# Kernel optimization log

Hardware: AMD Instinct MI355X
Metric: run time of the kernel (lower is better)

Reference implementation:

```python
import jax, jax.numpy as jnp
import numpy as np
import math

B, C, N = 8, 128, 16384
H = 4
DK = C // H
COUT = 128
EPS = 1e-5

def _ln(x, g, b):
    # x: (B,H,N,DK); g,b: (H,DK) -> per-head LayerNorm over last dim
    mu = jnp.mean(x, axis=-1, keepdims=True)
    var = jnp.mean((x - mu) ** 2, axis=-1, keepdims=True)
    xh = (x - mu) / jnp.sqrt(var + EPS)
    return xh * g[None, :, None, :] + b[None, :, None, :]

def setup_inputs() -> dict:
    key = jax.random.key(0)
    ks = jax.random.split(key, 12)
    s = 0.02
    return {
        "x": jax.random.normal(ks[0], (B, C, N), jnp.float32),
        "Wq": jax.random.normal(ks[1], (C, C), jnp.float32) * s + 0.01 * jnp.eye(C),
        "bq": jnp.zeros((C,), jnp.float32),
        "Wk": jax.random.normal(ks[2], (C, C), jnp.float32) * s + 0.01 * jnp.eye(C),
        "bk": jnp.zeros((C,), jnp.float32),
        "Wv": jax.random.normal(ks[3], (C, C), jnp.float32) * s + 0.01 * jnp.eye(C),
        "bv": jnp.zeros((C,), jnp.float32),
        "gK": jnp.ones((H, DK), jnp.float32),
        "bK": jnp.zeros((H, DK), jnp.float32),
        "gV": jnp.ones((H, DK), jnp.float32),
        "bV": jnp.zeros((H, DK), jnp.float32),
        "Wo": jax.random.normal(ks[4], (COUT, C), jnp.float32) * s,
        "bo": jnp.zeros((COUT,), jnp.float32),
    }

def reference(x, Wq, bq, Wk, bk, Wv, bv, gK, bK, gV, bV, Wo, bo):
    # x: (B, C, N) -> (B, N, C)
    xt = jnp.transpose(x, (0, 2, 1))
    def proj(W, b):
        y = xt @ W.T + b                      # (B,N,C)
        return jnp.transpose(y.reshape(B, N, H, DK), (0, 2, 1, 3))  # (B,H,N,DK)
    q = proj(Wq, bq)
    k = proj(Wk, bk)
    v = proj(Wv, bv)
    # galerkin: per-head LayerNorm on K and V (vectorized over heads)
    k = _ln(k, gK, bK)
    v = _ln(v, gV, bV)
    # linear (no-softmax) attention: (Q K^T / sqrt(dk)) / N @ V == Q @ (K^T V) / (sqrt(dk)*N)
    # dropout from F.dropout is treated as identity (deterministic reference)
    kv = jnp.einsum("bhnd,bhne->bhde", k, v)            # (B,H,DK,DK)
    attn = jnp.einsum("bhnd,bhde->bhne", q, kv) / (math.sqrt(DK) * N)
    out = jnp.transpose(attn, (0, 2, 1, 3)).reshape(B, N, C)  # merge heads
    out = out @ Wo.T + bo                                # (B,N,COUT)
    return jnp.transpose(out, (0, 2, 1))                 # (B,COUT,N)
```

## Files before the change

### kernel.cpp

```cpp
#include <hip/hip_runtime.h>
#include <cmath>

#define BB 8
#define CC 128
#define NN 16384
#define HH 4
#define TN 64
#define NT2 (NN / TN)
#define NBK 64
#define SX 272

typedef __attribute__((ext_vector_type(8))) short bf16x8;
typedef __attribute__((ext_vector_type(4))) float f32x4;

#define MFMA(a, b, c) __builtin_amdgcn_mfma_f32_16x16x32_bf16(a, b, c, 0, 0, 0)

__device__ __forceinline__ unsigned short f2b(float f) {
  union { float f; unsigned u; } v; v.f = f;
  unsigned r = v.u + 0x7FFFu + ((v.u >> 16) & 1u);
  return (unsigned short)(r >> 16);
}

__device__ __forceinline__ int xt_addr(int n, int cblk) {
  return n * SX + ((cblk ^ ((n >> 2) & 7)) << 4);
}
__device__ __forceinline__ int kt_byte(int c, int n) {
  return c * 144 + ((((n >> 3) ^ (c & 7)) << 4) | ((n & 7) << 1));
}

__global__ void k_prep(const float* __restrict__ Wq, const float* __restrict__ Wk,
                       const float* __restrict__ Wv, const float* __restrict__ Wo,
                       unsigned short* __restrict__ Wb) {
  const int idx = blockIdx.x * 256 + threadIdx.x;
  const int which = idx >> 14;
  const float* src = (which == 0) ? Wq : (which == 1) ? Wk : (which == 2) ? Wv : Wo;
  Wb[idx] = f2b(src[idx & 16383]);
}

__global__ __launch_bounds__(512, 4)
void k_fuse1(const float* __restrict__ x,
             const unsigned short* __restrict__ Wkb, const unsigned short* __restrict__ Wvb,
             const float* __restrict__ bk, const float* __restrict__ bv,
             const float* __restrict__ gK, const float* __restrict__ bK,
             const float* __restrict__ gV, const float* __restrict__ bV,
             float* __restrict__ kvp) {
  extern __shared__ char lds[];
  char* XT = lds;
  char* KT = lds + 34816;
  char* VT = lds + 53248;
  float* KVS = (float*)lds;

  const int tid = threadIdx.x;
  const int lane = tid & 63;
  const int w = tid >> 6;
  const int b = blockIdx.y;
  const int bx = blockIdx.x;
  const int l15 = lane & 15, l4 = lane >> 4;

  const int ph = w >> 1, pp = w & 1;
  const int kh = w >> 1, khalf = w & 1;

  const unsigned short* Wsrc = pp ? Wvb : Wkb;
  bf16x8 wf[2][4];
#pragma unroll
  for (int mf = 0; mf < 2; ++mf)
#pragma unroll
    for (int ks = 0; ks < 4; ++ks)
      wf[mf][ks] = *(const bf16x8*)(Wsrc + (ph * 32 + mf * 16 + l15) * 128 + ks * 32 + l4 * 8);

  float bias[2][4], gam[2][4], bet[2][4];
  {
    const float* bsrc = pp ? bv : bk;
    const float* gsrc = pp ? gV : gK;
    const float* esrc = pp ? bV : bK;
#pragma unroll
    for (int mf = 0; mf < 2; ++mf)
#pragma unroll
      for (int r = 0; r < 4; ++r) {
        const int cg = ph * 32 + mf * 16 + l4 * 4 + r;
        bias[mf][r] = bsrc[cg]; gam[mf][r] = gsrc[cg]; bet[mf][r] = esrc[cg];
      }
  }

  f32x4 kvacc[2][2];
#pragma unroll
  for (int i = 0; i < 2; ++i)
#pragma unroll
    for (int j = 0; j < 2; ++j) kvacc[i][j] = (f32x4){0.f, 0.f, 0.f, 0.f};

  for (int ot = 0; ot < 2; ++ot) {
    const int n0 = (bx * 2 + ot) * 128;

#pragma unroll
    for (int g = 0; g < 2; ++g) {
      const int cb = w * 2 + g;
      const float* xb = x + ((size_t)b * CC + cb * 8) * NN + n0 + lane * 2;
      float2 va[8];
#pragma unroll
      for (int cc = 0; cc < 8; ++cc) va[cc] = *(const float2*)(xb + (size_t)cc * NN);
#pragma unroll
      for (int j = 0; j < 2; ++j) {
        const int n = lane * 2 + j;
        bf16x8 pk;
#pragma unroll
        for (int cc = 0; cc < 8; ++cc)
          ((unsigned short*)&pk)[cc] = f2b(j ? va[cc].y : va[cc].x);
        *(bf16x8*)(XT + n * SX + ((cb ^ ((n >> 2) & 7)) << 4)) = pk;
      }
    }
    __syncthreads();

    for (int t = 0; t < 2; ++t) {
      const int nbase = t * 64;
      char* DST = pp ? VT : KT;
#pragma unroll
      for (int nf = 0; nf < 4; ++nf) {
        const int n = nbase + nf * 16 + l15;
        f32x4 a0 = (f32x4){0.f, 0.f, 0.f, 0.f}, a1 = (f32x4){0.f, 0.f, 0.f, 0.f};
#pragma unroll
        for (int ks = 0; ks < 4; ++ks) {
          const bf16x8 xf = *(const bf16x8*)(XT + xt_addr(n, ks * 4 + l4));
          a0 = MFMA(wf[0][ks], xf, a0);
          a1 = MFMA(wf[1][ks], xf, a1);
        }
#pragma unroll
        for (int r = 0; r < 4; ++r) { a0[r] += bias[0][r]; a1[r] += bias[1][r]; }
        float s = 0.f, ss = 0.f;
#pragma unroll
        for (int r = 0; r < 4; ++r) {
          s += a0[r] + a1[r];
          ss += a0[r] * a0[r] + a1[r] * a1[r];
        }
        s += __shfl_xor(s, 16); ss += __shfl_xor(ss, 16);
        s += __shfl_xor(s, 32); ss += __shfl_xor(ss, 32);
        const float mu = s * (1.f / 32.f);
        const float var = ss * (1.f / 32.f) - mu * mu;
        const float rstd = rsqrtf(var + 1e-5f);
        const int nloc = nf * 16 + l15;
#pragma unroll
        for (int r = 0; r < 4; ++r) {
          const int c0k = ph * 32 + l4 * 4 + r;
          *(unsigned short*)(DST + kt_byte(c0k, nloc)) =
              f2b((a0[r] - mu) * rstd * gam[0][r] + bet[0][r]);
          const int c1k = ph * 32 + 16 + l4 * 4 + r;
          *(unsigned short*)(DST + kt_byte(c1k, nloc)) =
              f2b((a1[r] - mu) * rstd * gam[1][r] + bet[1][r]);
        }
      }
      __syncthreads();

#pragma unroll
      for (int mf = 0; mf < 2; ++mf) {
        const int ck = kh * 32 + mf * 16 + l15;
        const bf16x8 ka = *(const bf16x8*)(KT + ck * 144 + (((khalf * 4 + l4) ^ (ck & 7)) << 4));
#pragma unroll
        for (int ef = 0; ef < 2; ++ef) {
          const int cv = kh * 32 + ef * 16 + l15;
          const bf16x8 vb = *(const bf16x8*)(VT + cv * 144 + (((khalf * 4 + l4) ^ (cv & 7)) << 4));
          kvacc[mf][ef] = MFMA(ka, vb, kvacc[mf][ef]);
        }
      }
      __syncthreads();
    }
  }

#pragma unroll
  for (int mf = 0; mf < 2; ++mf)
#pragma unroll
    for (int ef = 0; ef < 2; ++ef)
#pragma unroll
      for (int r = 0; r < 4; ++r) {
        const int d = mf * 16 + l4 * 4 + r, e = ef * 16 + l15;
        KVS[w * 1024 + d * 32 + e] = kvacc[mf][ef][r];
      }
  __syncthreads();
  {
    float* og = kvp + ((size_t)(b * NBK + bx)) * 8192;
#pragma unroll
    for (int i = 0; i < 4; ++i) {
      const int off = i * 2048 + tid * 4;
      *(f32x4*)(og + off) = *(const f32x4*)(KVS + off);
    }
  }
}

__global__ void k_reduceA(const float* __restrict__ kvp, float* __restrict__ p2) {
  const int blk = blockIdx.x;
  const int s = blk & 7, h = (blk >> 3) & 3, b = blk >> 5;
  const int t = threadIdx.x;
  f32x4 acc = (f32x4){0.f, 0.f, 0.f, 0.f};
  for (int i = 0; i < 8; ++i) {
    const int bx = s * 8 + i;
    const float* base = kvp + ((size_t)(b * NBK + bx)) * 8192 + t * 4;
    acc += *(const f32x4*)(base + (2 * h) * 1024);
    acc += *(const f32x4*)(base + (2 * h + 1) * 1024);
  }
  *(f32x4*)(p2 + (size_t)blk * 1024 + t * 4) = acc;
}

__global__ void k_reduceB(const float* __restrict__ p2, unsigned short* __restrict__ kvT,
                          const float scale) {
  const int bh = blockIdx.x;
  const int t = threadIdx.x;
  f32x4 acc = (f32x4){0.f, 0.f, 0.f, 0.f};
  for (int s = 0; s < 8; ++s)
    acc += *(const f32x4*)(p2 + ((size_t)bh * 8 + s) * 1024 + t * 4);
#pragma unroll
  for (int j = 0; j < 4; ++j) {
    const int i = t * 4 + j;
    const int d = i >> 5, e = i & 31;
    kvT[(size_t)bh * 1024 + e * 32 + d] = f2b(acc[j] * scale);
  }
}

__global__ __launch_bounds__(512, 4)
void k_pass2(const float* __restrict__ x,
             const unsigned short* __restrict__ Wqb, const float* __restrict__ bq,
             const unsigned short* __restrict__ kvT,
             const unsigned short* __restrict__ Wob, const float* __restrict__ bo,
             float* __restrict__ out) {
  extern __shared__ char lds[];
  char* XT = lds;
  char* QS = lds + 17408;
  char* AS = lds + 33792;
  float* OS = (float*)lds;

  const int tid = threadIdx.x;
  const int lane = tid & 63;
  const int w = tid >> 6;
  const int b = blockIdx.y;
  const int n0 = blockIdx.x * TN;
  const int l15 = lane & 15, l4 = lane >> 4;
  const int h = w >> 1, half = w & 1;

  bf16x8 kvf[2];
#pragma unroll
  for (int mf = 0; mf < 2; ++mf)
    kvf[mf] = *(const bf16x8*)(kvT + (((size_t)b * HH + h) * 32 + mf * 16 + l15) * 32 + l4 * 8);
  bf16x8 wq[4], wo[4];
#pragma unroll
  for (int ks = 0; ks < 4; ++ks) {
    wq[ks] = *(const bf16x8*)(Wqb + (w * 16 + l15) * 128 + ks * 32 + l4 * 8);
    wo[ks] = *(const bf16x8*)(Wob + (w * 16 + l15) * 128 + ks * 32 + l4 * 8);
  }
  float bq_r[4], bo_r[4];
#pragma unroll
  for (int r = 0; r < 4; ++r) {
    bq_r[r] = bq[w * 16 + l4 * 4 + r];
    bo_r[r] = bo[w * 16 + l4 * 4 + r];
  }

#pragma unroll
  for (int p = 0; p < 2; ++p) {
    const int cb = p * 8 + w;
    const float* xb = x + ((size_t)b * CC + cb * 8) * NN + n0 + lane;
    float va[8];
#pragma unroll
    for (int cc = 0; cc < 8; ++cc) va[cc] = xb[(size_t)cc * NN];
    bf16x8 pk;
#pragma unroll
    for (int cc = 0; cc < 8; ++cc) ((unsigned short*)&pk)[cc] = f2b(va[cc]);
    *(bf16x8*)(XT + lane * SX + ((cb ^ ((lane >> 2) & 7)) << 4)) = pk;
  }
  __syncthreads();

  f32x4 qa[4];
#pragma unroll
  for (int nf = 0; nf < 4; ++nf) qa[nf] = (f32x4){0.f, 0.f, 0.f, 0.f};
#pragma unroll
  for (int ks = 0; ks < 4; ++ks)
#pragma unroll
    for (int nf = 0; nf < 4; ++nf) {
      const int n = nf * 16 + l15;
      const bf16x8 xf = *(const bf16x8*)(XT + xt_addr(n, ks * 4 + l4));
      qa[nf] = MFMA(wq[ks], xf, qa[nf]);
    }
#pragma unroll
  for (int nf = 0; nf < 4; ++nf) {
    const int n = nf * 16 + l15;
    const int c0 = w * 16 + l4 * 4;
    unsigned long long pk = 0;
#pragma unroll
    for (int r = 0; r < 4; ++r)
      pk |= (unsigned long long)f2b(qa[nf][r] + bq_r[r]) << (16 * r);
    *(unsigned long long*)(QS + n * 256 + (((c0 >> 3) ^ (n & 15)) << 4) + ((c0 & 7) << 1)) = pk;
  }
  __syncthreads();

  f32x4 aa[2][2];
#pragma unroll
  for (int i = 0; i < 2; ++i)
#pragma unroll
    for (int j = 0; j < 2; ++j) aa[i][j] = (f32x4){0.f, 0.f, 0.f, 0.f};
  bf16x8 qf[2];
#pragma unroll
  for (int nf = 0; nf < 2; ++nf) {
    const int n = half * 32 + nf * 16 + l15;
    const int cq = h * 32 + l4 * 8;
    qf[nf] = *(const bf16x8*)(QS + n * 256 + ((((cq >> 3)) ^ (n & 15)) << 4));
  }
#pragma unroll
  for (int mf = 0; mf < 2; ++mf)
#pragma unroll
    for (int nf = 0; nf < 2; ++nf) aa[mf][nf] = MFMA(kvf[mf], qf[nf], aa[mf][nf]);
#pragma unroll
  for (int mf = 0; mf < 2; ++mf)
#pragma unroll
    for (int nf = 0; nf < 2; ++nf) {
      const int n = half * 32 + nf * 16 + l15;
      const int e0 = h * 32 + mf * 16 + l4 * 4;
      unsigned long long pk = 0;
#pragma unroll
      for (int r = 0; r < 4; ++r)
        pk |= (unsigned long long)f2b(aa[mf][nf][r]) << (16 * r);
      *(unsigned long long*)(AS + n * 256 + (((e0 >> 3) ^ (n & 15)) << 4) + ((e0 & 7) << 1)) = pk;
    }
  __syncthreads();

  f32x4 oa[4];
#pragma unroll
  for (int nf = 0; nf < 4; ++nf) oa[nf] = (f32x4){0.f, 0.f, 0.f, 0.f};
#pragma unroll
  for (int ks = 0; ks < 4; ++ks)
#pragma unroll
    for (int nf = 0; nf < 4; ++nf) {
      const int n = nf * 16 + l15;
      const bf16x8 af = *(const bf16x8*)(AS + n * 256 + (((ks * 4 + l4) ^ (n & 15)) << 4));
      oa[nf] = MFMA(wo[ks], af, oa[nf]);
    }
#pragma unroll
  for (int nf = 0; nf < 4; ++nf)
#pragma unroll
    for (int r = 0; r < 4; ++r)
      OS[(w * 16 + l4 * 4 + r) * 64 + nf * 16 + l15] = oa[nf][r] + bo_r[r];
  __syncthreads();

  {
    const int c = tid >> 2, seg = (tid & 3) * 16;
    const float* srcp = OS + c * 64 + seg;
    float* dstp = out + (size_t)b * CC * NN + (size_t)c * NN + n0 + seg;
#pragma unroll
    for (int j = 0; j < 4; ++j)
      ((float4*)dstp)[j] = ((const float4*)srcp)[j];
  }
}

extern "C" void kernel_launch(void* const* d_in, const int* in_sizes, int n_in,
                              void* d_out, int out_size, void* d_ws, size_t ws_size,
                              hipStream_t stream) {
  const float* x  = (const float*)d_in[0];
  const float* Wq = (const float*)d_in[1];
  const float* bq = (const float*)d_in[2];
  const float* Wk = (const float*)d_in[3];
  const float* bk = (const float*)d_in[4];
  const float* Wv = (const float*)d_in[5];
  const float* bv = (const float*)d_in[6];
  const float* gK = (const float*)d_in[7];
  const float* bK = (const float*)d_in[8];
  const float* gV = (const float*)d_in[9];
  const float* bV = (const float*)d_in[10];
  const float* Wo = (const float*)d_in[11];
  const float* bo = (const float*)d_in[12];
  float* out = (float*)d_out;

  char* ws = (char*)d_ws;
  float* kvp = (float*)ws;
  float* p2  = kvp + (size_t)BB * NBK * 8192;
  unsigned short* kvTb = (unsigned short*)(p2 + 256 * 1024);
  unsigned short* Wb = kvTb + (size_t)BB * HH * 1024;
  const unsigned short* Wqb = Wb;
  const unsigned short* Wkb = Wb + 16384;
  const unsigned short* Wvb = Wb + 32768;
  const unsigned short* Wob = Wb + 49152;

  (void)hipFuncSetAttribute(reinterpret_cast<const void*>(k_fuse1),
                            hipFuncAttributeMaxDynamicSharedMemorySize, 71680);
  (void)hipFuncSetAttribute(reinterpret_cast<const void*>(k_pass2),
                            hipFuncAttributeMaxDynamicSharedMemorySize, 50176);

  k_prep<<<256, 256, 0, stream>>>(Wq, Wk, Wv, Wo, Wb);

  k_fuse1<<<dim3(NBK, BB), 512, 71680, stream>>>(
      x, Wkb, Wvb, bk, bv, gK, bK, gV, bV, kvp);

  k_reduceA<<<256, 256, 0, stream>>>(kvp, p2);

  const float scale = 1.0f / (5.65685424949238f * 16384.0f);
  k_reduceB<<<32, 256, 0, stream>>>(p2, kvTb, scale);

  k_pass2<<<dim3(NT2, BB), 512, 50176, stream>>>(
      x, Wqb, bq, kvTb, Wob, bo, out);
}
```

Before: 87.96 us.

## Register-prefetch x tiles with double-buffered LDS in fuse1 and persistent pass2

Both k_fuse1 and k_pass2 now loop over four 64-column tiles per block, loading the next tile of x into registers while the current one is converted and computed, and alternating between two LDS staging buffers. k_pass2 moves from 256 blocks per batch at 64 columns to 64 blocks at 256 columns, and it writes the output straight from MFMA registers rather than staging it through LDS for coalesced float4 stores. The goal is to hide global load latency and cut barriers and per-block setup. The cost is fewer blocks, more LDS per block, and output stores that are less coalesced.

```diff
diff --git a/kernel.cpp b/kernel.cpp
--- a/kernel.cpp
+++ b/kernel.cpp
@@ -5,8 +5,6 @@
 #define CC 128
 #define NN 16384
 #define HH 4
-#define TN 64
-#define NT2 (NN / TN)
 #define NBK 64
 #define SX 272
 
@@ -45,7 +43,6 @@
              const float* __restrict__ gV, const float* __restrict__ bV,
              float* __restrict__ kvp) {
   extern __shared__ char lds[];
-  char* XT = lds;
   char* KT = lds + 34816;
   char* VT = lds + 53248;
   float* KVS = (float*)lds;
@@ -88,82 +85,84 @@
 #pragma unroll
     for (int j = 0; j < 2; ++j) kvacc[i][j] = (f32x4){0.f, 0.f, 0.f, 0.f};
 
-  for (int ot = 0; ot < 2; ++ot) {
-    const int n0 = (bx * 2 + ot) * 128;
-
-#pragma unroll
-    for (int g = 0; g < 2; ++g) {
-      const int cb = w * 2 + g;
-      const float* xb = x + ((size_t)b * CC + cb * 8) * NN + n0 + lane * 2;
-      float2 va[8];
-#pragma unroll
-      for (int cc = 0; cc < 8; ++cc) va[cc] = *(const float2*)(xb + (size_t)cc * NN);
-#pragma unroll
-      for (int j = 0; j < 2; ++j) {
-        const int n = lane * 2 + j;
-        bf16x8 pk;
-#pragma unroll
-        for (int cc = 0; cc < 8; ++cc)
-          ((unsigned short*)&pk)[cc] = f2b(j ? va[cc].y : va[cc].x);
-        *(bf16x8*)(XT + n * SX + ((cb ^ ((n >> 2) & 7)) << 4)) = pk;
-      }
-    }
-    __syncthreads();
-
-    for (int t = 0; t < 2; ++t) {
-      const int nbase = t * 64;
-      char* DST = pp ? VT : KT;
-#pragma unroll
-      for (int nf = 0; nf < 4; ++nf) {
-        const int n = nbase + nf * 16 + l15;
-        f32x4 a0 = (f32x4){0.f, 0.f, 0.f, 0.f}, a1 = (f32x4){0.f, 0.f, 0.f, 0.f};
-#pragma unroll
-        for (int ks = 0; ks < 4; ++ks) {
-          const bf16x8 xf = *(const bf16x8*)(XT + xt_addr(n, ks * 4 + l4));
-          a0 = MFMA(wf[0][ks], xf, a0);
-          a1 = MFMA(wf[1][ks], xf, a1);
-        }
-#pragma unroll
-        for (int r = 0; r < 4; ++r) { a0[r] += bias[0][r]; a1[r] += bias[1][r]; }
-        float s = 0.f, ss = 0.f;
-#pragma unroll
-        for (int r = 0; r < 4; ++r) {
-          s += a0[r] + a1[r];
-          ss += a0[r] * a0[r] + a1[r] * a1[r];
-        }
-        s += __shfl_xor(s, 16); ss += __shfl_xor(ss, 16);
-        s += __shfl_xor(s, 32); ss += __shfl_xor(ss, 32);
-        const float mu = s * (1.f / 32.f);
-        const float var = ss * (1.f / 32.f) - mu * mu;
-        const float rstd = rsqrtf(var + 1e-5f);
-        const int nloc = nf * 16 + l15;
-#pragma unroll
-        for (int r = 0; r < 4; ++r) {
-          const int c0k = ph * 32 + l4 * 4 + r;
-          *(unsigned short*)(DST + kt_byte(c0k, nloc)) =
-              f2b((a0[r] - mu) * rstd * gam[0][r] + bet[0][r]);
-          const int c1k = ph * 32 + 16 + l4 * 4 + r;
-          *(unsigned short*)(DST + kt_byte(c1k, nloc)) =
-              f2b((a1[r] - mu) * rstd * gam[1][r] + bet[1][r]);
-        }
-      }
-      __syncthreads();
-
-#pragma unroll
-      for (int mf = 0; mf < 2; ++mf) {
-        const int ck = kh * 32 + mf * 16 + l15;
-        const bf16x8 ka = *(const bf16x8*)(KT + ck * 144 + (((khalf * 4 + l4) ^ (ck & 7)) << 4));
-#pragma unroll
-        for (int ef = 0; ef < 2; ++ef) {
-          const int cv = kh * 32 + ef * 16 + l15;
-          const bf16x8 vb = *(const bf16x8*)(VT + cv * 144 + (((khalf * 4 + l4) ^ (cv & 7)) << 4));
-          kvacc[mf][ef] = MFMA(ka, vb, kvacc[mf][ef]);
-        }
-      }
-      __syncthreads();
-    }
-  }
-
+  const int half2 = lane >> 5;
+  const int cb2 = w * 2 + half2;
+  const int nn = (lane & 31) * 2;
+  const float* xrow = x + ((size_t)b * CC + cb2 * 8) * NN + bx * 256 + nn;
+
+  float2 rx[8];
+#pragma unroll
+  for (int cc = 0; cc < 8; ++cc) rx[cc] = *(const float2*)(xrow + (size_t)cc * NN);
+
+  for (int it = 0; it < 4; ++it) {
+    char* XT = (it & 1) ? (lds + 17408) : lds;
+
+#pragma unroll
+    for (int j = 0; j < 2; ++j) {
+      const int n = nn + j;
+      bf16x8 pk;
+#pragma unroll
+      for (int cc = 0; cc < 8; ++cc)
+        ((unsigned short*)&pk)[cc] = f2b(j ? rx[cc].y : rx[cc].x);
+      *(bf16x8*)(XT + n * SX + ((cb2 ^ ((n >> 2) & 7)) << 4)) = pk;
+    }
+    if (it < 3) {
+      const float* xn = xrow + (it + 1) * 64;
+#pragma unroll
+      for (int cc = 0; cc < 8; ++cc) rx[cc] = *(const float2*)(xn + (size_t)cc * NN);
+    }
+    __syncthreads();
+
+    char* DST = pp ? VT : KT;
+#pragma unroll
+    for (int nf = 0; nf < 4; ++nf) {
+      const int n = nf * 16 + l15;
+      f32x4 a0 = (f32x4){0.f, 0.f, 0.f, 0.f}, a1 = (f32x4){0.f, 0.f, 0.f, 0.f};
+#pragma unroll
+      for (int ks = 0; ks < 4; ++ks) {
+        const bf16x8 xf = *(const bf16x8*)(XT + xt_addr(n, ks * 4 + l4));
+        a0 = MFMA(wf[0][ks], xf, a0);
+        a1 = MFMA(wf[1][ks], xf, a1);
+      }
+#pragma unroll
+      for (int r = 0; r < 4; ++r) { a0[r] += bias[0][r]; a1[r] += bias[1][r]; }
+      float s = 0.f, ss = 0.f;
+#pragma unroll
+      for (int r = 0; r < 4; ++r) {
+        s += a0[r] + a1[r];
+        ss += a0[r] * a0[r] + a1[r] * a1[r];
+      }
+      s += __shfl_xor(s, 16); ss += __shfl_xor(ss, 16);
+      s += __shfl_xor(s, 32); ss += __shfl_xor(ss, 32);
+      const float mu = s * (1.f / 32.f);
+      const float var = ss * (1.f / 32.f) - mu * mu;
+      const float rstd = rsqrtf(var + 1e-5f);
+#pragma unroll
+      for (int r = 0; r < 4; ++r) {
+        const int c0k = ph * 32 + l4 * 4 + r;
+        *(unsigned short*)(DST + kt_byte(c0k, n)) =
+            f2b((a0[r] - mu) * rstd * gam[0][r] + bet[0][r]);
+        const int c1k = ph * 32 + 16 + l4 * 4 + r;
+        *(unsigned short*)(DST + kt_byte(c1k, n)) =
+            f2b((a1[r] - mu) * rstd * gam[1][r] + bet[1][r]);
+      }
+    }
+    __syncthreads();
+
+#pragma unroll
+    for (int mf = 0; mf < 2; ++mf) {
+      const int ck = kh * 32 + mf * 16 + l15;
+      const bf16x8 ka = *(const bf16x8*)(KT + ck * 144 + (((khalf * 4 + l4) ^ (ck & 7)) << 4));
+#pragma unroll
+      for (int ef = 0; ef < 2; ++ef) {
+        const int cv = kh * 32 + ef * 16 + l15;
+        const bf16x8 vb = *(const bf16x8*)(VT + cv * 144 + (((khalf * 4 + l4) ^ (cv & 7)) << 4));
+        kvacc[mf][ef] = MFMA(ka, vb, kvacc[mf][ef]);
+      }
+    }
+  }
+
+  __syncthreads();
 #pragma unroll
   for (int mf = 0; mf < 2; ++mf)
 #pragma unroll
@@ -220,16 +219,13 @@
              const unsigned short* __restrict__ Wob, const float* __restrict__ bo,
              float* __restrict__ out) {
   extern __shared__ char lds[];
-  char* XT = lds;
-  char* QS = lds + 17408;
-  char* AS = lds + 33792;
-  float* OS = (float*)lds;
+  char* QS = lds + 34816;
+  char* AS = lds + 51200;
 
   const int tid = threadIdx.x;
   const int lane = tid & 63;
   const int w = tid >> 6;
   const int b = blockIdx.y;
-  const int n0 = blockIdx.x * TN;
   const int l15 = lane & 15, l4 = lane >> 4;
   const int h = w >> 1, half = w & 1;
 
@@ -250,98 +246,107 @@
     bo_r[r] = bo[w * 16 + l4 * 4 + r];
   }
 
-#pragma unroll
-  for (int p = 0; p < 2; ++p) {
-    const int cb = p * 8 + w;
-    const float* xb = x + ((size_t)b * CC + cb * 8) * NN + n0 + lane;
-    float va[8];
-#pragma unroll
-    for (int cc = 0; cc < 8; ++cc) va[cc] = xb[(size_t)cc * NN];
-    bf16x8 pk;
-#pragma unroll
-    for (int cc = 0; cc < 8; ++cc) ((unsigned short*)&pk)[cc] = f2b(va[cc]);
-    *(bf16x8*)(XT + lane * SX + ((cb ^ ((lane >> 2) & 7)) << 4)) = pk;
-  }
-  __syncthreads();
-
-  f32x4 qa[4];
-#pragma unroll
-  for (int nf = 0; nf < 4; ++nf) qa[nf] = (f32x4){0.f, 0.f, 0.f, 0.f};
-#pragma unroll
-  for (int ks = 0; ks < 4; ++ks)
+  const int half2 = lane >> 5;
+  const int cb2 = w * 2 + half2;
+  const int nn = (lane & 31) * 2;
+  const float* xrow = x + ((size_t)b * CC + cb2 * 8) * NN + blockIdx.x * 256 + nn;
+  float* ob = out + (size_t)b * CC * NN;
+
+  float2 rx[8];
+#pragma unroll
+  for (int cc = 0; cc < 8; ++cc) rx[cc] = *(const float2*)(xrow + (size_t)cc * NN);
+
+  for (int it = 0; it < 4; ++it) {
+    const int n0 = blockIdx.x * 256 + it * 64;
+    char* XT = (it & 1) ? (lds + 17408) : lds;
+
+#pragma unroll
+    for (int j = 0; j < 2; ++j) {
+      const int n = nn + j;
+      bf16x8 pk;
+#pragma unroll
+      for (int cc = 0; cc < 8; ++cc)
+        ((unsigned short*)&pk)[cc] = f2b(j ? rx[cc].y : rx[cc].x);
+      *(bf16x8*)(XT + n * SX + ((cb2 ^ ((n >> 2) & 7)) << 4)) = pk;
+    }
+    if (it < 3) {
+      const float* xn = xrow + (it + 1) * 64;
+#pragma unroll
+      for (int cc = 0; cc < 8; ++cc) rx[cc] = *(const float2*)(xn + (size_t)cc * NN);
+    }
+    __syncthreads();
+
+    f32x4 qa[4];
+#pragma unroll
+    for (int nf = 0; nf < 4; ++nf) qa[nf] = (f32x4){0.f, 0.f, 0.f, 0.f};
+#pragma unroll
+    for (int ks = 0; ks < 4; ++ks)
+#pragma unroll
+      for (int nf = 0; nf < 4; ++nf) {
+        const int n = nf * 16 + l15;
+        const bf16x8 xf = *(const bf16x8*)(XT + xt_addr(n, ks * 4 + l4));
+        qa[nf] = MFMA(wq[ks], xf, qa[nf]);
+      }
 #pragma unroll
     for (int nf = 0; nf < 4; ++nf) {
       const int n = nf * 16 + l15;
-      const bf16x8 xf = *(const bf16x8*)(XT + xt_addr(n, ks * 4 + l4));
-      qa[nf] = MFMA(wq[ks], xf, qa[nf]);
-    }
-#pragma unroll
-  for (int nf = 0; nf < 4; ++nf) {
-    const int n = nf * 16 + l15;
-    const int c0 = w * 16 + l4 * 4;
-    unsigned long long pk = 0;
-#pragma unroll
-    for (int r = 0; r < 4; ++r)
-      pk |= (unsigned long long)f2b(qa[nf][r] + bq_r[r]) << (16 * r);
-    *(unsigned long long*)(QS + n * 256 + (((c0 >> 3) ^ (n & 15)) << 4) + ((c0 & 7) << 1)) = pk;
-  }
-  __syncthreads();
-
-  f32x4 aa[2][2];
-#pragma unroll
-  for (int i = 0; i < 2; ++i)
-#pragma unroll
-    for (int j = 0; j < 2; ++j) aa[i][j] = (f32x4){0.f, 0.f, 0.f, 0.f};
-  bf16x8 qf[2];
-#pragma unroll
-  for (int nf = 0; nf < 2; ++nf) {
-    const int n = half * 32 + nf * 16 + l15;
-    const int cq = h * 32 + l4 * 8;
-    qf[nf] = *(const bf16x8*)(QS + n * 256 + ((((cq >> 3)) ^ (n & 15)) << 4));
-  }
-#pragma unroll
-  for (int mf = 0; mf < 2; ++mf)
-#pragma unroll
-    for (int nf = 0; nf < 2; ++nf) aa[mf][nf] = MFMA(kvf[mf], qf[nf], aa[mf][nf]);
-#pragma unroll
-  for (int mf = 0; mf < 2; ++mf)
+      const int c0 = w * 16 + l4 * 4;
+      unsigned long long pk = 0;
+#pragma unroll
+      for (int r = 0; r < 4; ++r)
+        pk |= (unsigned long long)f2b(qa[nf][r] + bq_r[r]) << (16 * r);
+      *(unsigned long long*)(QS + n * 256 + (((c0 >> 3) ^ (n & 15)) << 4) + ((c0 & 7) << 1)) = pk;
+    }
+    __syncthreads();
+
+    f32x4 aa[2][2];
+#pragma unroll
+    for (int i = 0; i < 2; ++i)
+#pragma unroll
+      for (int j = 0; j < 2; ++j) aa[i][j] = (f32x4){0.f, 0.f, 0.f, 0.f};
+    bf16x8 qf[2];
 #pragma unroll
     for (int nf = 0; nf < 2; ++nf) {
       const int n = half * 32 + nf * 16 + l15;
-      const int e0 = h * 32 + mf * 16 + l4 * 4;
-      unsigned long long pk = 0;
-#pragma unroll
-      for (int r = 0; r < 4; ++r)
-        pk |= (unsigned long long)f2b(aa[mf][nf][r]) << (16 * r);
-      *(unsigned long long*)(AS + n * 256 + (((e0 >> 3) ^ (n & 15)) << 4) + ((e0 & 7) << 1)) = pk;
-    }
-  __syncthreads();
-
-  f32x4 oa[4];
-#pragma unroll
-  for (int nf = 0; nf < 4; ++nf) oa[nf] = (f32x4){0.f, 0.f, 0.f, 0.f};
-#pragma unroll
-  for (int ks = 0; ks < 4; ++ks)
-#pragma unroll
-    for (int nf = 0; nf < 4; ++nf) {
-      const int n = nf * 16 + l15;
-      const bf16x8 af = *(const bf16x8*)(AS + n * 256 + (((ks * 4 + l4) ^ (n & 15)) << 4));
-      oa[nf] = MFMA(wo[ks], af, oa[nf]);
-    }
-#pragma unroll
-  for (int nf = 0; nf < 4; ++nf)
-#pragma unroll
-    for (int r = 0; r < 4; ++r)
-      OS[(w * 16 + l4 * 4 + r) * 64 + nf * 16 + l15] = oa[nf][r] + bo_r[r];
-  __syncthreads();
-
-  {
-    const int c = tid >> 2, seg = (tid & 3) * 16;
-    const float* srcp = OS + c * 64 + seg;
-    float* dstp = out + (size_t)b * CC * NN + (size_t)c * NN + n0 + seg;
-#pragma unroll
-    for (int j = 0; j < 4; ++j)
-      ((float4*)dstp)[j] = ((const float4*)srcp)[j];
+      const int cq = h * 32 + l4 * 8;
+      qf[nf] = *(const bf16x8*)(QS + n * 256 + ((((cq >> 3)) ^ (n & 15)) << 4));
+    }
+#pragma unroll
+    for (int mf = 0; mf < 2; ++mf)
+#pragma unroll
+      for (int nf = 0; nf < 2; ++nf) aa[mf][nf] = MFMA(kvf[mf], qf[nf], aa[mf][nf]);
+#pragma unroll
+    for (int mf = 0; mf < 2; ++mf)
+#pragma unroll
+      for (int nf = 0; nf < 2; ++nf) {
+        const int n = half * 32 + nf * 16 + l15;
+        const int e0 = h * 32 + mf * 16 + l4 * 4;
+        unsigned long long pk = 0;
+#pragma unroll
+        for (int r = 0; r < 4; ++r)
+          pk |= (unsigned long long)f2b(aa[mf][nf][r]) << (16 * r);
+        *(unsigned long long*)(AS + n * 256 + (((e0 >> 3) ^ (n & 15)) << 4) + ((e0 & 7) << 1)) = pk;
+      }
+    __syncthreads();
+
+    f32x4 oa[4];
+#pragma unroll
+    for (int nf = 0; nf < 4; ++nf) oa[nf] = (f32x4){0.f, 0.f, 0.f, 0.f};
+#pragma unroll
+    for (int ks = 0; ks < 4; ++ks)
+#pragma unroll
+      for (int nf = 0; nf < 4; ++nf) {
+        const int n = nf * 16 + l15;
+        const bf16x8 af = *(const bf16x8*)(AS + n * 256 + (((ks * 4 + l4) ^ (n & 15)) << 4));
+        oa[nf] = MFMA(wo[ks], af, oa[nf]);
+      }
+#pragma unroll
+    for (int nf = 0; nf < 4; ++nf)
+#pragma unroll
+      for (int r = 0; r < 4; ++r) {
+        const int c = w * 16 + l4 * 4 + r;
+        ob[(size_t)c * NN + n0 + nf * 16 + l15] = oa[nf][r] + bo_r[r];
+      }
   }
 }
 
@@ -376,7 +381,7 @@
   (void)hipFuncSetAttribute(reinterpret_cast<const void*>(k_fuse1),
                             hipFuncAttributeMaxDynamicSharedMemorySize, 71680);
   (void)hipFuncSetAttribute(reinterpret_cast<const void*>(k_pass2),
-                            hipFuncAttributeMaxDynamicSharedMemorySize, 50176);
+                            hipFuncAttributeMaxDynamicSharedMemorySize, 67584);
 
   k_prep<<<256, 256, 0, stream>>>(Wq, Wk, Wv, Wo, Wb);
 
@@ -388,6 +393,6 @@
   const float scale = 1.0f / (5.65685424949238f * 16384.0f);
   k_reduceB<<<32, 256, 0, stream>>>(p2, kvTb, scale);
 
-  k_pass2<<<dim3(NT2, BB), 512, 50176, stream>>>(
+  k_pass2<<<dim3(NBK, BB), 512, 67584, stream>>>(
       x, Wqb, bq, kvTb, Wob, bo, out);
 }
```

New measurement: 81.52 us. -7.3%, faster.

## Compute Q projection in pass-one kernel and stream bf16 Q to pass two

Applied to the files above, without the earlier changes.

Moves the Q projection into the first fused kernel, which already stages x in LDS, and writes Q as bf16 to a workspace buffer. The second kernel no longer re-reads and converts fp32 x. It loads Q directly, processes four column tiles per block with double-buffered LDS, and stores output straight to global memory. This trades the second fp32 read of x for a bf16 write plus read of Q, and adds MFMA work to the first kernel.

```diff
diff --git a/kernel.cpp b/kernel.cpp
--- a/kernel.cpp
+++ b/kernel.cpp
@@ -5,8 +5,6 @@
 #define CC 128
 #define NN 16384
 #define HH 4
-#define TN 64
-#define NT2 (NN / TN)
 #define NBK 64
 #define SX 272
 
@@ -39,11 +37,12 @@
 
 __global__ __launch_bounds__(512, 4)
 void k_fuse1(const float* __restrict__ x,
+             const unsigned short* __restrict__ Wqb, const float* __restrict__ bq,
              const unsigned short* __restrict__ Wkb, const unsigned short* __restrict__ Wvb,
              const float* __restrict__ bk, const float* __restrict__ bv,
              const float* __restrict__ gK, const float* __restrict__ bK,
              const float* __restrict__ gV, const float* __restrict__ bV,
-             float* __restrict__ kvp) {
+             unsigned short* __restrict__ qg, float* __restrict__ kvp) {
   extern __shared__ char lds[];
   char* XT = lds;
   char* KT = lds + 34816;
@@ -68,6 +67,14 @@
     for (int ks = 0; ks < 4; ++ks)
       wf[mf][ks] = *(const bf16x8*)(Wsrc + (ph * 32 + mf * 16 + l15) * 128 + ks * 32 + l4 * 8);
 
+  bf16x8 wq[4];
+#pragma unroll
+  for (int ks = 0; ks < 4; ++ks)
+    wq[ks] = *(const bf16x8*)(Wqb + (w * 16 + l15) * 128 + ks * 32 + l4 * 8);
+  float bq_r[4];
+#pragma unroll
+  for (int r = 0; r < 4; ++r) bq_r[r] = bq[w * 16 + l4 * 4 + r];
+
   float bias[2][4], gam[2][4], bet[2][4];
   {
     const float* bsrc = pp ? bv : bk;
@@ -88,6 +95,9 @@
 #pragma unroll
     for (int j = 0; j < 2; ++j) kvacc[i][j] = (f32x4){0.f, 0.f, 0.f, 0.f};
 
+  unsigned short* qchunk =
+      qg + (((size_t)(b * HH + (w >> 1)) * 4 + (w & 1) * 2 + (l4 >> 1)) * NN) * 8 + (l4 & 1) * 4;
+
   for (int ot = 0; ot < 2; ++ot) {
     const int n0 = (bx * 2 + ot) * 128;
 
@@ -112,6 +122,26 @@
 
     for (int t = 0; t < 2; ++t) {
       const int nbase = t * 64;
+
+      {
+        unsigned short* qb = qchunk + (size_t)(n0 + nbase) * 8;
+#pragma unroll
+        for (int nf = 0; nf < 4; ++nf) {
+          const int n = nbase + nf * 16 + l15;
+          f32x4 qa = (f32x4){0.f, 0.f, 0.f, 0.f};
+#pragma unroll
+          for (int ks = 0; ks < 4; ++ks) {
+            const bf16x8 xf = *(const bf16x8*)(XT + xt_addr(n, ks * 4 + l4));
+            qa = MFMA(wq[ks], xf, qa);
+          }
+          unsigned long long pk = 0;
+#pragma unroll
+          for (int r = 0; r < 4; ++r)
+            pk |= (unsigned long long)f2b(qa[r] + bq_r[r]) << (16 * r);
+          *(unsigned long long*)(qb + (size_t)(nf * 16 + l15) * 8) = pk;
+        }
+      }
+
       char* DST = pp ? VT : KT;
 #pragma unroll
       for (int nf = 0; nf < 4; ++nf) {
@@ -213,23 +243,18 @@
   }
 }
 
-__global__ __launch_bounds__(512, 4)
-void k_pass2(const float* __restrict__ x,
-             const unsigned short* __restrict__ Wqb, const float* __restrict__ bq,
+__global__ __launch_bounds__(512, 6)
+void k_pass2(const unsigned short* __restrict__ qg,
              const unsigned short* __restrict__ kvT,
              const unsigned short* __restrict__ Wob, const float* __restrict__ bo,
              float* __restrict__ out) {
   extern __shared__ char lds[];
-  char* XT = lds;
-  char* QS = lds + 17408;
-  char* AS = lds + 33792;
-  float* OS = (float*)lds;
 
   const int tid = threadIdx.x;
   const int lane = tid & 63;
   const int w = tid >> 6;
   const int b = blockIdx.y;
-  const int n0 = blockIdx.x * TN;
+  const int bx = blockIdx.x;
   const int l15 = lane & 15, l4 = lane >> 4;
   const int h = w >> 1, half = w & 1;
 
@@ -237,111 +262,66 @@
 #pragma unroll
   for (int mf = 0; mf < 2; ++mf)
     kvf[mf] = *(const bf16x8*)(kvT + (((size_t)b * HH + h) * 32 + mf * 16 + l15) * 32 + l4 * 8);
-  bf16x8 wq[4], wo[4];
-#pragma unroll
-  for (int ks = 0; ks < 4; ++ks) {
-    wq[ks] = *(const bf16x8*)(Wqb + (w * 16 + l15) * 128 + ks * 32 + l4 * 8);
+  bf16x8 wo[4];
+#pragma unroll
+  for (int ks = 0; ks < 4; ++ks)
     wo[ks] = *(const bf16x8*)(Wob + (w * 16 + l15) * 128 + ks * 32 + l4 * 8);
-  }
-  float bq_r[4], bo_r[4];
-#pragma unroll
-  for (int r = 0; r < 4; ++r) {
-    bq_r[r] = bq[w * 16 + l4 * 4 + r];
-    bo_r[r] = bo[w * 16 + l4 * 4 + r];
-  }
-
-#pragma unroll
-  for (int p = 0; p < 2; ++p) {
-    const int cb = p * 8 + w;
-    const float* xb = x + ((size_t)b * CC + cb * 8) * NN + n0 + lane;
-    float va[8];
-#pragma unroll
-    for (int cc = 0; cc < 8; ++cc) va[cc] = xb[(size_t)cc * NN];
-    bf16x8 pk;
-#pragma unroll
-    for (int cc = 0; cc < 8; ++cc) ((unsigned short*)&pk)[cc] = f2b(va[cc]);
-    *(bf16x8*)(XT + lane * SX + ((cb ^ ((lane >> 2) & 7)) << 4)) = pk;
-  }
-  __syncthreads();
-
-  f32x4 qa[4];
-#pragma unroll
-  for (int nf = 0; nf < 4; ++nf) qa[nf] = (f32x4){0.f, 0.f, 0.f, 0.f};
-#pragma unroll
-  for (int ks = 0; ks < 4; ++ks)
-#pragma unroll
-    for (int nf = 0; nf < 4; ++nf) {
-      const int n = nf * 16 + l15;
-      const bf16x8 xf = *(const bf16x8*)(XT + xt_addr(n, ks * 4 + l4));
-      qa[nf] = MFMA(wq[ks], xf, qa[nf]);
-    }
-#pragma unroll
-  for (int nf = 0; nf < 4; ++nf) {
-    const int n = nf * 16 + l15;
-    const int c0 = w * 16 + l4 * 4;
-    unsigned long long pk = 0;
-#pragma unroll
-    for (int r = 0; r < 4; ++r)
-      pk |= (unsigned long long)f2b(qa[nf][r] + bq_r[r]) << (16 * r);
-    *(unsigned long long*)(QS + n * 256 + (((c0 >> 3) ^ (n & 15)) << 4) + ((c0 & 7) << 1)) = pk;
-  }
-  __syncthreads();
-
-  f32x4 aa[2][2];
-#pragma unroll
-  for (int i = 0; i < 2; ++i)
-#pragma unroll
-    for (int j = 0; j < 2; ++j) aa[i][j] = (f32x4){0.f, 0.f, 0.f, 0.f};
-  bf16x8 qf[2];
-#pragma unroll
-  for (int nf = 0; nf < 2; ++nf) {
-    const int n = half * 32 + nf * 16 + l15;
-    const int cq = h * 32 + l4 * 8;
-    qf[nf] = *(const bf16x8*)(QS + n * 256 + ((((cq >> 3)) ^ (n & 15)) << 4));
-  }
-#pragma unroll
-  for (int mf = 0; mf < 2; ++mf)
-#pragma unroll
-    for (int nf = 0; nf < 2; ++nf) aa[mf][nf] = MFMA(kvf[mf], qf[nf], aa[mf][nf]);
-#pragma unroll
-  for (int mf = 0; mf < 2; ++mf)
-#pragma unroll
-    for (int nf = 0; nf < 2; ++nf) {
-      const int n = half * 32 + nf * 16 + l15;
-      const int e0 = h * 32 + mf * 16 + l4 * 4;
-      unsigned long long pk = 0;
-#pragma unroll
-      for (int r = 0; r < 4; ++r)
-        pk |= (unsigned long long)f2b(aa[mf][nf][r]) << (16 * r);
-      *(unsigned long long*)(AS + n * 256 + (((e0 >> 3) ^ (n & 15)) << 4) + ((e0 & 7) << 1)) = pk;
-    }
-  __syncthreads();
-
-  f32x4 oa[4];
-#pragma unroll
-  for (int nf = 0; nf < 4; ++nf) oa[nf] = (f32x4){0.f, 0.f, 0.f, 0.f};
-#pragma unroll
-  for (int ks = 0; ks < 4; ++ks)
-#pragma unroll
-    for (int nf = 0; nf < 4; ++nf) {
-      const int n = nf * 16 + l15;
-      const bf16x8 af = *(const bf16x8*)(AS + n * 256 + (((ks * 4 + l4) ^ (n & 15)) << 4));
-      oa[nf] = MFMA(wo[ks], af, oa[nf]);
-    }
-#pragma unroll
-  for (int nf = 0; nf < 4; ++nf)
-#pragma unroll
-    for (int r = 0; r < 4; ++r)
-      OS[(w * 16 + l4 * 4 + r) * 64 + nf * 16 + l15] = oa[nf][r] + bo_r[r];
-  __syncthreads();
-
-  {
-    const int c = tid >> 2, seg = (tid & 3) * 16;
-    const float* srcp = OS + c * 64 + seg;
-    float* dstp = out + (size_t)b * CC * NN + (size_t)c * NN + n0 + seg;
-#pragma unroll
-    for (int j = 0; j < 4; ++j)
-      ((float4*)dstp)[j] = ((const float4*)srcp)[j];
+  float bo_r[4];
+#pragma unroll
+  for (int r = 0; r < 4; ++r) bo_r[r] = bo[w * 16 + l4 * 4 + r];
+
+  const unsigned short* qbase = qg + (((size_t)(b * HH + h) * 4 + l4) * NN) * 8;
+  float* ob = out + (size_t)b * CC * NN;
+
+  for (int it = 0; it < 4; ++it) {
+    const int n0 = bx * 256 + it * 64;
+    char* AS = lds + (it & 1) * 16384;
+
+    bf16x8 qf[2];
+#pragma unroll
+    for (int nf = 0; nf < 2; ++nf)
+      qf[nf] = *(const bf16x8*)(qbase + (size_t)(n0 + half * 32 + nf * 16 + l15) * 8);
+    f32x4 aa[2][2];
+#pragma unroll
+    for (int i = 0; i < 2; ++i)
+#pragma unroll
+      for (int j = 0; j < 2; ++j) aa[i][j] = (f32x4){0.f, 0.f, 0.f, 0.f};
+#pragma unroll
+    for (int mf = 0; mf < 2; ++mf)
+#pragma unroll
+      for (int nf = 0; nf < 2; ++nf) aa[mf][nf] = MFMA(kvf[mf], qf[nf], aa[mf][nf]);
+#pragma unroll
+    for (int mf = 0; mf < 2; ++mf)
+#pragma unroll
+      for (int nf = 0; nf < 2; ++nf) {
+        const int n = half * 32 + nf * 16 + l15;
+        const int e0 = h * 32 + mf * 16 + l4 * 4;
+        unsigned long long pk = 0;
+#pragma unroll
+        for (int r = 0; r < 4; ++r)
+          pk |= (unsigned long long)f2b(aa[mf][nf][r]) << (16 * r);
+        *(unsigned long long*)(AS + n * 256 + (((e0 >> 3) ^ (n & 15)) << 4) + ((e0 & 7) << 1)) = pk;
+      }
+    __syncthreads();
+
+    f32x4 oa[4];
+#pragma unroll
+    for (int nf = 0; nf < 4; ++nf) oa[nf] = (f32x4){0.f, 0.f, 0.f, 0.f};
+#pragma unroll
+    for (int ks = 0; ks < 4; ++ks)
+#pragma unroll
+      for (int nf = 0; nf < 4; ++nf) {
+        const int n = nf * 16 + l15;
+        const bf16x8 af = *(const bf16x8*)(AS + n * 256 + (((ks * 4 + l4) ^ (n & 15)) << 4));
+        oa[nf] = MFMA(wo[ks], af, oa[nf]);
+      }
+#pragma unroll
+    for (int nf = 0; nf < 4; ++nf)
+#pragma unroll
+      for (int r = 0; r < 4; ++r) {
+        const int c = w * 16 + l4 * 4 + r;
+        ob[(size_t)c * NN + n0 + nf * 16 + l15] = oa[nf][r] + bo_r[r];
+      }
   }
 }
 
@@ -368,6 +348,7 @@
   float* p2  = kvp + (size_t)BB * NBK * 8192;
   unsigned short* kvTb = (unsigned short*)(p2 + 256 * 1024);
   unsigned short* Wb = kvTb + (size_t)BB * HH * 1024;
+  unsigned short* qg = Wb + 65536;
   const unsigned short* Wqb = Wb;
   const unsigned short* Wkb = Wb + 16384;
   const unsigned short* Wvb = Wb + 32768;
@@ -376,18 +357,18 @@
   (void)hipFuncSetAttribute(reinterpret_cast<const void*>(k_fuse1),
                             hipFuncAttributeMaxDynamicSharedMemorySize, 71680);
   (void)hipFuncSetAttribute(reinterpret_cast<const void*>(k_pass2),
-                            hipFuncAttributeMaxDynamicSharedMemorySize, 50176);
+                            hipFuncAttributeMaxDynamicSharedMemorySize, 32768);
 
   k_prep<<<256, 256, 0, stream>>>(Wq, Wk, Wv, Wo, Wb);
 
   k_fuse1<<<dim3(NBK, BB), 512, 71680, stream>>>(
-      x, Wkb, Wvb, bk, bv, gK, bK, gV, bV, kvp);
+      x, Wqb, bq, Wkb, Wvb, bk, bv, gK, bK, gV, bV, qg, kvp);
 
   k_reduceA<<<256, 256, 0, stream>>>(kvp, p2);
 
   const float scale = 1.0f / (5.65685424949238f * 16384.0f);
   k_reduceB<<<32, 256, 0, stream>>>(p2, kvTb, scale);
 
-  k_pass2<<<dim3(NT2, BB), 512, 50176, stream>>>(
-      x, Wqb, bq, kvTb, Wob, bo, out);
-}
+  k_pass2<<<dim3(NBK, BB), 512, 32768, stream>>>(
+      qg, kvTb, Wob, bo, out);
+}
```

New measurement: 139.0 us. 1.58x slower.
